# Kernel tuning notes

Hardware: AMD Instinct MI355X
Metric: run time of the kernel (lower is better)

The kernel has to match this reference:

```python
import jax, jax.numpy as jnp
import numpy as np

N_RAYS, N_SAMPLES = 65536, 128


def setup_inputs() -> dict:
    key = jax.random.key(0)
    ks = jax.random.split(key, 6)
    sdf = jax.random.normal(ks[0], (N_RAYS, N_SAMPLES), dtype=jnp.float32)
    color = jax.random.uniform(ks[1], (N_RAYS, N_SAMPLES, 3), dtype=jnp.float32)
    # strictly increasing positive depths per ray
    dz = jax.random.uniform(ks[2], (N_RAYS, N_SAMPLES), dtype=jnp.float32) * 0.05 + 0.01
    z_vals = 0.1 + jnp.cumsum(dz, axis=-1)
    grad_theta = jax.random.normal(ks[3], (N_RAYS, N_SAMPLES, 3), dtype=jnp.float32)
    rd = jax.random.normal(ks[4], (N_RAYS, 3), dtype=jnp.float32)
    rays_d = rd / jnp.linalg.norm(rd, axis=-1, keepdims=True)
    s = jnp.array([64.0], dtype=jnp.float32)  # inv_s from SingleVarianceNetwork
    cos_anneal_ratio = jnp.float32(0.5)
    return {"sdf": sdf, "color": color, "z_vals": z_vals,
            "grad_theta": grad_theta, "rays_d": rays_d, "s": s,
            "cos_anneal_ratio": cos_anneal_ratio}


def reference(sdf, color, z_vals, grad_theta, rays_d, s, cos_anneal_ratio):
    # true cosine between ray dir and SDF gradient: [N, S]
    true_cos = jnp.sum(rays_d[:, None, :] * grad_theta, axis=-1)
    # annealed non-positive cosine (NeuS cos annealing)
    iter_cos = -(jax.nn.relu(-true_cos * 0.5 + 0.5) * (1.0 - cos_anneal_ratio)
                 + jax.nn.relu(-true_cos) * cos_anneal_ratio)
    dists = z_vals[:, 1:] - z_vals[:, :-1]                 # [N, S-1]
    est_next_sdf = sdf[..., :-1] + iter_cos[..., :-1] * dists * 0.5
    est_prev_sdf = sdf[..., :-1] - iter_cos[..., :-1] * dists * 0.5
    sv = s.reshape(())                                     # scalar inv_s
    prev_cdf = jax.nn.sigmoid(est_prev_sdf * sv)
    next_cdf = jax.nn.sigmoid(est_next_sdf * sv)
    alpha = jnp.clip((prev_cdf - next_cdf + 1e-5) / (prev_cdf + 1e-5), 0.0, 1.0)
    transmittance = jnp.cumprod(1.0 - alpha, axis=-1)      # [N, S-1]
    # faithful to source: a ZERO column is prepended to transmittance
    zcol = jnp.zeros((transmittance.shape[0], 1), transmittance.dtype)
    transmittance = jnp.concatenate([zcol, transmittance], axis=-1)  # [N, S]
    alpha = jnp.clip(jnp.concatenate([alpha, zcol], axis=-1), 0.0, 1.0)
    weight = transmittance * alpha                          # [N, S]
    pixel = jnp.sum(weight[..., None] * color, axis=-2)     # [N, 3]
    invdepth = jnp.sum(weight / z_vals, axis=-1)            # [N]
    return pixel, invdepth, weight
```

## Files before the change

### kernel.cpp

```cpp
#include <hip/hip_runtime.h>

#define N_RAYS 65536
#define N_SAMPLES 128
#define RPB 8

__device__ __forceinline__ void gll16(const float* g, float* l) {
    __builtin_amdgcn_global_load_lds(
        (const __attribute__((address_space(1))) void*)g,
        (__attribute__((address_space(3))) void*)l,
        16, 0, 0);
}

__device__ __forceinline__ float sigmoidf(float x) {
    return __fdividef(1.0f, 1.0f + __expf(-x));
}

__global__ __launch_bounds__(256, 8) void neus_kernel(
    const float* __restrict__ sdf,
    const float* __restrict__ color,
    const float* __restrict__ z_vals,
    const float* __restrict__ grad_theta,
    const float* __restrict__ rays_d,
    const float* __restrict__ s_ptr,
    const float* __restrict__ car_ptr,
    float* __restrict__ out_pixel,
    float* __restrict__ out_invdepth,
    float* __restrict__ out_weight)
{
    __shared__ __align__(16) float lds[RPB * N_SAMPLES * 3];

    const int tid = threadIdx.x;
    const int l   = tid & 31;
    const int r   = tid >> 5;
    const int wv  = tid >> 6;
    const int l64 = tid & 63;
    const int ray = blockIdx.x * RPB + r;

    const size_t base  = (size_t)ray * N_SAMPLES;
    const size_t base3 = (size_t)blockIdx.x * (RPB * N_SAMPLES * 3);

    {
        const float* g = grad_theta + base3;
        #pragma unroll
        for (int k = 0; k < 3; ++k) {
            const int q = wv * 3 + k;
            gll16(g + q * 256 + l64 * 4, &lds[q * 256]);
        }
    }

    const float4 sd = *(const float4*)(sdf    + base + 4 * l);
    const float4 zz = *(const float4*)(z_vals + base + 4 * l);
    const float rdx = rays_d[ray * 3 + 0];
    const float rdy = rays_d[ray * 3 + 1];
    const float rdz = rays_d[ray * 3 + 2];
    const float sv  = s_ptr[0];
    const float car = car_ptr[0];
    const float omc = 1.0f - car;

    asm volatile("s_waitcnt vmcnt(0)" ::: "memory");

    const int fo = r * 384 + 12 * l;
    const float4 gA = *(const float4*)&lds[fo + 0];
    const float4 gB = *(const float4*)&lds[fo + 4];
    const float4 gC = *(const float4*)&lds[fo + 8];

    asm volatile("s_waitcnt lgkmcnt(0)" ::: "memory");

    {
        const float* c = color + base3;
        #pragma unroll
        for (int k = 0; k < 3; ++k) {
            const int q = wv * 3 + k;
            gll16(c + q * 256 + l64 * 4, &lds[q * 256]);
        }
    }

    const float tc0 = rdx * gA.x + rdy * gA.y + rdz * gA.z;
    const float tc1 = rdx * gA.w + rdy * gB.x + rdz * gB.y;
    const float tc2 = rdx * gB.z + rdy * gB.w + rdz * gC.x;
    const float tc3 = rdx * gC.y + rdy * gC.z + rdz * gC.w;

    auto iter_cos = [&](float tc) -> float {
        float a = fmaxf(fmaf(tc, -0.5f, 0.5f), 0.0f);
        float b = fmaxf(-tc, 0.0f);
        return -(a * omc + b * car);
    };
    const float ic0 = iter_cos(tc0);
    const float ic1 = iter_cos(tc1);
    const float ic2 = iter_cos(tc2);
    const float ic3 = iter_cos(tc3);

    const float zn = __shfl_down(zz.x, 1, 32);
    const float d0 = zz.y - zz.x;
    const float d1 = zz.z - zz.y;
    const float d2 = zz.w - zz.z;
    const float d3 = zn   - zz.w;

    auto alpha_f = [&](float sdv, float ic, float d) -> float {
        float h  = ic * d * 0.5f;
        float pc = sigmoidf((sdv - h) * sv);
        float nc = sigmoidf((sdv + h) * sv);
        float a  = __fdividef(pc - nc + 1e-5f, pc + 1e-5f);
        return fminf(fmaxf(a, 0.0f), 1.0f);
    };
    const float a0 = alpha_f(sd.x, ic0, d0);
    const float a1 = alpha_f(sd.y, ic1, d1);
    const float a2 = alpha_f(sd.z, ic2, d2);
    const float a3 = (l == 31) ? 0.0f : alpha_f(sd.w, ic3, d3);

    const float om0 = 1.0f - a0;
    const float om1 = 1.0f - a1;
    const float om2 = 1.0f - a2;
    const float om3 = 1.0f - a3;

    float scan = om0 * om1 * om2 * om3;
    #pragma unroll
    for (int off = 1; off < 32; off <<= 1) {
        float v = __shfl_up(scan, off, 32);
        if (l >= off) scan *= v;
    }
    float excl = __shfl_up(scan, 1, 32);
    if (l == 0) excl = 1.0f;

    float t  = excl;
    const float w0 = (l == 0) ? 0.0f : t * a0;
    t *= om0; const float w1 = t * a1;
    t *= om1; const float w2 = t * a2;
    t *= om2; const float w3 = t * a3;

    float inv = w0 * __fdividef(1.0f, zz.x) + w1 * __fdividef(1.0f, zz.y)
              + w2 * __fdividef(1.0f, zz.z) + w3 * __fdividef(1.0f, zz.w);

    asm volatile("s_waitcnt vmcnt(0)" ::: "memory");

    const float4 cA = *(const float4*)&lds[fo + 0];
    const float4 cB = *(const float4*)&lds[fo + 4];
    const float4 cC = *(const float4*)&lds[fo + 8];

    *(float4*)(out_weight + base + 4 * l) = make_float4(w0, w1, w2, w3);

    float pr = w0 * cA.x + w1 * cA.w + w2 * cB.z + w3 * cC.y;
    float pg = w0 * cA.y + w1 * cB.x + w2 * cB.w + w3 * cC.z;
    float pb = w0 * cA.z + w1 * cB.y + w2 * cC.x + w3 * cC.w;

    #pragma unroll
    for (int off = 16; off > 0; off >>= 1) {
        pr  += __shfl_xor(pr,  off, 32);
        pg  += __shfl_xor(pg,  off, 32);
        pb  += __shfl_xor(pb,  off, 32);
        inv += __shfl_xor(inv, off, 32);
    }

    if (l == 0) {
        out_pixel[ray * 3 + 0] = pr;
        out_pixel[ray * 3 + 1] = pg;
        out_pixel[ray * 3 + 2] = pb;
        out_invdepth[ray]      = inv;
    }
}

extern "C" void kernel_launch(void* const* d_in, const int* in_sizes, int n_in,
                              void* d_out, int out_size, void* d_ws, size_t ws_size,
                              hipStream_t stream) {
    const float* sdf        = (const float*)d_in[0];
    const float* color      = (const float*)d_in[1];
    const float* z_vals     = (const float*)d_in[2];
    const float* grad_theta = (const float*)d_in[3];
    const float* rays_d     = (const float*)d_in[4];
    const float* s_ptr      = (const float*)d_in[5];
    const float* car_ptr    = (const float*)d_in[6];

    float* out          = (float*)d_out;
    float* out_pixel    = out;
    float* out_invdepth = out + (size_t)N_RAYS * 3;
    float* out_weight   = out + (size_t)N_RAYS * 4;

    dim3 block(256);
    dim3 grid(N_RAYS / RPB);

    neus_kernel<<<grid, block, 0, stream>>>(
        sdf, color, z_vals, grad_theta, rays_d, s_ptr, car_ptr,
        out_pixel, out_invdepth, out_weight);
}
```

Baseline: 273.8 us.

## Convert to persistent grid with double-buffered LDS prefetch of grad and color

Replaces the one-block-per-8-rays launch with a fixed grid of 768 persistent blocks that loop over ray tiles. While one tile is computed, the next tile's grad_theta and color are prefetched into a second LDS buffer, along with its sdf and z_vals in registers. rays_d is staged into LDS once up front. This aims to hide global-load latency behind compute, at the cost of lower occupancy (launch bounds drop to 3 blocks) and a larger LDS footprint. Fast divisions are also swapped for regular IEEE divisions, which adds ALU cost.

Result: slower. 283.0 us (+3.4%).

```diff
diff --git a/kernel.cpp b/kernel.cpp
--- a/kernel.cpp
+++ b/kernel.cpp
@@ -1,8 +1,12 @@
 #include <hip/hip_runtime.h>
 
-#define N_RAYS 65536
+#define N_RAYS   65536
 #define N_SAMPLES 128
-#define RPB 8
+#define RPT      8
+#define GRID     768
+#define NTG      (N_RAYS / RPT)
+#define MAXT     ((NTG + GRID - 1) / GRID)
+#define TILE_F   (RPT * N_SAMPLES * 3)
 
 __device__ __forceinline__ void gll16(const float* g, float* l) {
     __builtin_amdgcn_global_load_lds(
@@ -12,10 +16,23 @@
 }
 
 __device__ __forceinline__ float sigmoidf(float x) {
-    return __fdividef(1.0f, 1.0f + __expf(-x));
-}
-
-__global__ __launch_bounds__(256, 8) void neus_kernel(
+    return 1.0f / (1.0f + __expf(-x));
+}
+
+__device__ __forceinline__ void stage(const float* __restrict__ grad,
+                                      const float* __restrict__ color,
+                                      float* b, int wv, int l64, size_t rayb) {
+    const float* g = grad  + rayb * (N_SAMPLES * 3);
+    const float* c = color + rayb * (N_SAMPLES * 3);
+    #pragma unroll
+    for (int k = 0; k < 3; ++k) {
+        const int q = wv * 3 + k;
+        gll16(g + (size_t)q * 256 + l64 * 4, b + q * 256);
+        gll16(c + (size_t)q * 256 + l64 * 4, b + TILE_F + q * 256);
+    }
+}
+
+__global__ __launch_bounds__(256, 3) void neus_kernel(
     const float* __restrict__ sdf,
     const float* __restrict__ color,
     const float* __restrict__ z_vals,
@@ -27,135 +44,143 @@
     float* __restrict__ out_invdepth,
     float* __restrict__ out_weight)
 {
-    __shared__ __align__(16) float lds[RPB * N_SAMPLES * 3];
+    __shared__ __align__(16) float buf[2][TILE_F * 2];
+    __shared__ float lds_rd[MAXT * RPT * 3];
 
     const int tid = threadIdx.x;
     const int l   = tid & 31;
-    const int r   = tid >> 5;
+    const int rl  = tid >> 5;
     const int wv  = tid >> 6;
     const int l64 = tid & 63;
-    const int ray = blockIdx.x * RPB + r;
-
-    const size_t base  = (size_t)ray * N_SAMPLES;
-    const size_t base3 = (size_t)blockIdx.x * (RPB * N_SAMPLES * 3);
-
-    {
-        const float* g = grad_theta + base3;
-        #pragma unroll
-        for (int k = 0; k < 3; ++k) {
-            const int q = wv * 3 + k;
-            gll16(g + q * 256 + l64 * 4, &lds[q * 256]);
-        }
+    const int bid = blockIdx.x;
+
+    const int ntiles = (NTG - bid + GRID - 1) / GRID;
+
+    const int nrd = ntiles * RPT * 3;
+    for (int k = tid; k < nrd; k += 256) {
+        const int it  = k / 24;
+        const int rem = k - it * 24;
+        lds_rd[k] = rays_d[(size_t)(bid + it * GRID) * 24 + rem];
     }
 
-    const float4 sd = *(const float4*)(sdf    + base + 4 * l);
-    const float4 zz = *(const float4*)(z_vals + base + 4 * l);
-    const float rdx = rays_d[ray * 3 + 0];
-    const float rdy = rays_d[ray * 3 + 1];
-    const float rdz = rays_d[ray * 3 + 2];
     const float sv  = s_ptr[0];
     const float car = car_ptr[0];
     const float omc = 1.0f - car;
 
-    asm volatile("s_waitcnt vmcnt(0)" ::: "memory");
-
-    const int fo = r * 384 + 12 * l;
-    const float4 gA = *(const float4*)&lds[fo + 0];
-    const float4 gB = *(const float4*)&lds[fo + 4];
-    const float4 gC = *(const float4*)&lds[fo + 8];
-
-    asm volatile("s_waitcnt lgkmcnt(0)" ::: "memory");
-
-    {
-        const float* c = color + base3;
+    __syncthreads();
+
+    size_t tg = bid;
+    int parity = 0;
+    stage(grad_theta, color, buf[0], wv, l64, tg * RPT);
+    float4 sdP = *(const float4*)(sdf    + (tg * RPT + rl) * N_SAMPLES + 4 * l);
+    float4 zzP = *(const float4*)(z_vals + (tg * RPT + rl) * N_SAMPLES + 4 * l);
+
+    for (int i = 0; ; ++i) {
+        const size_t tg_next = tg + GRID;
+        const bool   more    = (i + 1) < ntiles;
+        float4 sdN, zzN;
+        if (more) {
+            stage(grad_theta, color, buf[parity ^ 1], wv, l64, tg_next * RPT);
+            sdN = *(const float4*)(sdf    + (tg_next * RPT + rl) * N_SAMPLES + 4 * l);
+            zzN = *(const float4*)(z_vals + (tg_next * RPT + rl) * N_SAMPLES + 4 * l);
+            asm volatile("s_waitcnt vmcnt(8)" ::: "memory");
+        } else {
+            asm volatile("s_waitcnt vmcnt(0)" ::: "memory");
+        }
+
+        const float* bb = buf[parity];
+        const int fo = rl * 384 + 12 * l;
+        const float4 gA = *(const float4*)(bb + fo);
+        const float4 gB = *(const float4*)(bb + fo + 4);
+        const float4 gC = *(const float4*)(bb + fo + 8);
+        const float4 cA = *(const float4*)(bb + TILE_F + fo);
+        const float4 cB = *(const float4*)(bb + TILE_F + fo + 4);
+        const float4 cC = *(const float4*)(bb + TILE_F + fo + 8);
+        const float rdx = lds_rd[i * 24 + rl * 3 + 0];
+        const float rdy = lds_rd[i * 24 + rl * 3 + 1];
+        const float rdz = lds_rd[i * 24 + rl * 3 + 2];
+        asm volatile("s_waitcnt lgkmcnt(0)" ::: "memory");
+
+        const float tc0 = rdx * gA.x + rdy * gA.y + rdz * gA.z;
+        const float tc1 = rdx * gA.w + rdy * gB.x + rdz * gB.y;
+        const float tc2 = rdx * gB.z + rdy * gB.w + rdz * gC.x;
+        const float tc3 = rdx * gC.y + rdy * gC.z + rdz * gC.w;
+
+        auto iter_cos = [&](float tc) -> float {
+            float a = fmaxf(fmaf(tc, -0.5f, 0.5f), 0.0f);
+            float b = fmaxf(-tc, 0.0f);
+            return -(a * omc + b * car);
+        };
+        const float ic0 = iter_cos(tc0);
+        const float ic1 = iter_cos(tc1);
+        const float ic2 = iter_cos(tc2);
+        const float ic3 = iter_cos(tc3);
+
+        const float zn = __shfl_down(zzP.x, 1, 32);
+        const float d0 = zzP.y - zzP.x;
+        const float d1 = zzP.z - zzP.y;
+        const float d2 = zzP.w - zzP.z;
+        const float d3 = zn    - zzP.w;
+
+        auto alpha_f = [&](float sdv, float ic, float d) -> float {
+            float h  = ic * d * 0.5f;
+            float pc = sigmoidf((sdv - h) * sv);
+            float nc = sigmoidf((sdv + h) * sv);
+            float a  = (pc - nc + 1e-5f) / (pc + 1e-5f);
+            return fminf(fmaxf(a, 0.0f), 1.0f);
+        };
+        const float a0 = alpha_f(sdP.x, ic0, d0);
+        const float a1 = alpha_f(sdP.y, ic1, d1);
+        const float a2 = alpha_f(sdP.z, ic2, d2);
+        const float a3 = (l == 31) ? 0.0f : alpha_f(sdP.w, ic3, d3);
+
+        const float om0 = 1.0f - a0;
+        const float om1 = 1.0f - a1;
+        const float om2 = 1.0f - a2;
+        const float om3 = 1.0f - a3;
+
+        float scan = om0 * om1 * om2 * om3;
         #pragma unroll
-        for (int k = 0; k < 3; ++k) {
-            const int q = wv * 3 + k;
-            gll16(c + q * 256 + l64 * 4, &lds[q * 256]);
-        }
-    }
-
-    const float tc0 = rdx * gA.x + rdy * gA.y + rdz * gA.z;
-    const float tc1 = rdx * gA.w + rdy * gB.x + rdz * gB.y;
-    const float tc2 = rdx * gB.z + rdy * gB.w + rdz * gC.x;
-    const float tc3 = rdx * gC.y + rdy * gC.z + rdz * gC.w;
-
-    auto iter_cos = [&](float tc) -> float {
-        float a = fmaxf(fmaf(tc, -0.5f, 0.5f), 0.0f);
-        float b = fmaxf(-tc, 0.0f);
-        return -(a * omc + b * car);
-    };
-    const float ic0 = iter_cos(tc0);
-    const float ic1 = iter_cos(tc1);
-    const float ic2 = iter_cos(tc2);
-    const float ic3 = iter_cos(tc3);
-
-    const float zn = __shfl_down(zz.x, 1, 32);
-    const float d0 = zz.y - zz.x;
-    const float d1 = zz.z - zz.y;
-    const float d2 = zz.w - zz.z;
-    const float d3 = zn   - zz.w;
-
-    auto alpha_f = [&](float sdv, float ic, float d) -> float {
-        float h  = ic * d * 0.5f;
-        float pc = sigmoidf((sdv - h) * sv);
-        float nc = sigmoidf((sdv + h) * sv);
-        float a  = __fdividef(pc - nc + 1e-5f, pc + 1e-5f);
-        return fminf(fmaxf(a, 0.0f), 1.0f);
-    };
-    const float a0 = alpha_f(sd.x, ic0, d0);
-    const float a1 = alpha_f(sd.y, ic1, d1);
-    const float a2 = alpha_f(sd.z, ic2, d2);
-    const float a3 = (l == 31) ? 0.0f : alpha_f(sd.w, ic3, d3);
-
-    const float om0 = 1.0f - a0;
-    const float om1 = 1.0f - a1;
-    const float om2 = 1.0f - a2;
-    const float om3 = 1.0f - a3;
-
-    float scan = om0 * om1 * om2 * om3;
-    #pragma unroll
-    for (int off = 1; off < 32; off <<= 1) {
-        float v = __shfl_up(scan, off, 32);
-        if (l >= off) scan *= v;
-    }
-    float excl = __shfl_up(scan, 1, 32);
-    if (l == 0) excl = 1.0f;
-
-    float t  = excl;
-    const float w0 = (l == 0) ? 0.0f : t * a0;
-    t *= om0; const float w1 = t * a1;
-    t *= om1; const float w2 = t * a2;
-    t *= om2; const float w3 = t * a3;
-
-    float inv = w0 * __fdividef(1.0f, zz.x) + w1 * __fdividef(1.0f, zz.y)
-              + w2 * __fdividef(1.0f, zz.z) + w3 * __fdividef(1.0f, zz.w);
-
-    asm volatile("s_waitcnt vmcnt(0)" ::: "memory");
-
-    const float4 cA = *(const float4*)&lds[fo + 0];
-    const float4 cB = *(const float4*)&lds[fo + 4];
-    const float4 cC = *(const float4*)&lds[fo + 8];
-
-    *(float4*)(out_weight + base + 4 * l) = make_float4(w0, w1, w2, w3);
-
-    float pr = w0 * cA.x + w1 * cA.w + w2 * cB.z + w3 * cC.y;
-    float pg = w0 * cA.y + w1 * cB.x + w2 * cB.w + w3 * cC.z;
-    float pb = w0 * cA.z + w1 * cB.y + w2 * cC.x + w3 * cC.w;
-
-    #pragma unroll
-    for (int off = 16; off > 0; off >>= 1) {
-        pr  += __shfl_xor(pr,  off, 32);
-        pg  += __shfl_xor(pg,  off, 32);
-        pb  += __shfl_xor(pb,  off, 32);
-        inv += __shfl_xor(inv, off, 32);
-    }
-
-    if (l == 0) {
-        out_pixel[ray * 3 + 0] = pr;
-        out_pixel[ray * 3 + 1] = pg;
-        out_pixel[ray * 3 + 2] = pb;
-        out_invdepth[ray]      = inv;
+        for (int off = 1; off < 32; off <<= 1) {
+            float v = __shfl_up(scan, off, 32);
+            if (l >= off) scan *= v;
+        }
+        float excl = __shfl_up(scan, 1, 32);
+        if (l == 0) excl = 1.0f;
+
+        float t  = excl;
+        const float w0 = (l == 0) ? 0.0f : t * a0;
+        t *= om0; const float w1 = t * a1;
+        t *= om1; const float w2 = t * a2;
+        t *= om2; const float w3 = t * a3;
+
+        float inv = w0 / zzP.x + w1 / zzP.y + w2 / zzP.z + w3 / zzP.w;
+
+        const size_t ray  = tg * RPT + rl;
+        const size_t base = ray * N_SAMPLES;
+        *(float4*)(out_weight + base + 4 * l) = make_float4(w0, w1, w2, w3);
+
+        float pr = w0 * cA.x + w1 * cA.w + w2 * cB.z + w3 * cC.y;
+        float pg = w0 * cA.y + w1 * cB.x + w2 * cB.w + w3 * cC.z;
+        float pb = w0 * cA.z + w1 * cB.y + w2 * cC.x + w3 * cC.w;
+
+        #pragma unroll
+        for (int off = 16; off > 0; off >>= 1) {
+            pr  += __shfl_xor(pr,  off, 32);
+            pg  += __shfl_xor(pg,  off, 32);
+            pb  += __shfl_xor(pb,  off, 32);
+            inv += __shfl_xor(inv, off, 32);
+        }
+
+        if (l == 0) {
+            out_pixel[ray * 3 + 0] = pr;
+            out_pixel[ray * 3 + 1] = pg;
+            out_pixel[ray * 3 + 2] = pb;
+            out_invdepth[ray]      = inv;
+        }
+
+        if (!more) break;
+        sdP = sdN; zzP = zzN; tg = tg_next; parity ^= 1;
     }
 }
 
@@ -176,7 +201,7 @@
     float* out_weight   = out + (size_t)N_RAYS * 4;
 
     dim3 block(256);
-    dim3 grid(N_RAYS / RPB);
+    dim3 grid(GRID);
 
     neus_kernel<<<grid, block, 0, stream>>>(
         sdf, color, z_vals, grad_theta, rays_d, s_ptr, car_ptr,
```

## Replace LDS-staged global_load_lds with direct vector loads of grad and color

Applied to the files above, without the earlier changes.

Drops the LDS staging of grad_theta and color, along with the explicit waitcnt barriers. Each lane now issues three 16-byte global loads directly from its own 48-byte segment, and grad_theta uses nontemporal loads. All loads are issued up front, so color traffic overlaps the compute. The launch-bounds occupancy hint is removed, and fast divides are swapped for IEEE divides, which adds ALU cost. Direct per-lane loads of a 48-byte stride are less coalesced per instruction than the contiguous LDS copy.

Measured after the change: 261.9 us. -4.3%, faster.

```diff
diff --git a/kernel.cpp b/kernel.cpp
--- a/kernel.cpp
+++ b/kernel.cpp
@@ -1,21 +1,22 @@
 #include <hip/hip_runtime.h>
 
-#define N_RAYS 65536
+#define N_RAYS   65536
 #define N_SAMPLES 128
-#define RPB 8
 
-__device__ __forceinline__ void gll16(const float* g, float* l) {
-    __builtin_amdgcn_global_load_lds(
-        (const __attribute__((address_space(1))) void*)g,
-        (__attribute__((address_space(3))) void*)l,
-        16, 0, 0);
+typedef float f4 __attribute__((ext_vector_type(4)));
+
+__device__ __forceinline__ f4 ntload4(const float* p) {
+    return __builtin_nontemporal_load((const f4*)p);
+}
+__device__ __forceinline__ f4 load4(const float* p) {
+    return *(const f4*)p;
 }
 
 __device__ __forceinline__ float sigmoidf(float x) {
-    return __fdividef(1.0f, 1.0f + __expf(-x));
+    return 1.0f / (1.0f + __expf(-x));
 }
 
-__global__ __launch_bounds__(256, 8) void neus_kernel(
+__global__ __launch_bounds__(256) void neus_kernel(
     const float* __restrict__ sdf,
     const float* __restrict__ color,
     const float* __restrict__ z_vals,
@@ -27,53 +28,31 @@
     float* __restrict__ out_invdepth,
     float* __restrict__ out_weight)
 {
-    __shared__ __align__(16) float lds[RPB * N_SAMPLES * 3];
-
     const int tid = threadIdx.x;
     const int l   = tid & 31;
-    const int r   = tid >> 5;
-    const int wv  = tid >> 6;
-    const int l64 = tid & 63;
-    const int ray = blockIdx.x * RPB + r;
+    const int rl  = tid >> 5;
+    const int ray = blockIdx.x * 8 + rl;
 
-    const size_t base  = (size_t)ray * N_SAMPLES;
-    const size_t base3 = (size_t)blockIdx.x * (RPB * N_SAMPLES * 3);
+    const size_t base = (size_t)ray * N_SAMPLES;
+    const size_t b3   = base * 3 + 12 * l;
 
-    {
-        const float* g = grad_theta + base3;
-        #pragma unroll
-        for (int k = 0; k < 3; ++k) {
-            const int q = wv * 3 + k;
-            gll16(g + q * 256 + l64 * 4, &lds[q * 256]);
-        }
-    }
+    const f4 sd = load4(sdf    + base + 4 * l);
+    const f4 zz = load4(z_vals + base + 4 * l);
 
-    const float4 sd = *(const float4*)(sdf    + base + 4 * l);
-    const float4 zz = *(const float4*)(z_vals + base + 4 * l);
+    const f4 gA = ntload4(grad_theta + b3);
+    const f4 gB = ntload4(grad_theta + b3 + 4);
+    const f4 gC = ntload4(grad_theta + b3 + 8);
+
+    const f4 cA = load4(color + b3);
+    const f4 cB = load4(color + b3 + 4);
+    const f4 cC = load4(color + b3 + 8);
+
     const float rdx = rays_d[ray * 3 + 0];
     const float rdy = rays_d[ray * 3 + 1];
     const float rdz = rays_d[ray * 3 + 2];
     const float sv  = s_ptr[0];
     const float car = car_ptr[0];
     const float omc = 1.0f - car;
-
-    asm volatile("s_waitcnt vmcnt(0)" ::: "memory");
-
-    const int fo = r * 384 + 12 * l;
-    const float4 gA = *(const float4*)&lds[fo + 0];
-    const float4 gB = *(const float4*)&lds[fo + 4];
-    const float4 gC = *(const float4*)&lds[fo + 8];
-
-    asm volatile("s_waitcnt lgkmcnt(0)" ::: "memory");
-
-    {
-        const float* c = color + base3;
-        #pragma unroll
-        for (int k = 0; k < 3; ++k) {
-            const int q = wv * 3 + k;
-            gll16(c + q * 256 + l64 * 4, &lds[q * 256]);
-        }
-    }
 
     const float tc0 = rdx * gA.x + rdy * gA.y + rdz * gA.z;
     const float tc1 = rdx * gA.w + rdy * gB.x + rdz * gB.y;
@@ -100,7 +79,7 @@
         float h  = ic * d * 0.5f;
         float pc = sigmoidf((sdv - h) * sv);
         float nc = sigmoidf((sdv + h) * sv);
-        float a  = __fdividef(pc - nc + 1e-5f, pc + 1e-5f);
+        float a  = (pc - nc + 1e-5f) / (pc + 1e-5f);
         return fminf(fmaxf(a, 0.0f), 1.0f);
     };
     const float a0 = alpha_f(sd.x, ic0, d0);
@@ -128,16 +107,10 @@
     t *= om1; const float w2 = t * a2;
     t *= om2; const float w3 = t * a3;
 
-    float inv = w0 * __fdividef(1.0f, zz.x) + w1 * __fdividef(1.0f, zz.y)
-              + w2 * __fdividef(1.0f, zz.z) + w3 * __fdividef(1.0f, zz.w);
+    float inv = w0 / zz.x + w1 / zz.y + w2 / zz.z + w3 / zz.w;
 
-    asm volatile("s_waitcnt vmcnt(0)" ::: "memory");
-
-    const float4 cA = *(const float4*)&lds[fo + 0];
-    const float4 cB = *(const float4*)&lds[fo + 4];
-    const float4 cC = *(const float4*)&lds[fo + 8];
-
-    *(float4*)(out_weight + base + 4 * l) = make_float4(w0, w1, w2, w3);
+    f4 wv; wv.x = w0; wv.y = w1; wv.z = w2; wv.w = w3;
+    *(f4*)(out_weight + base + 4 * l) = wv;
 
     float pr = w0 * cA.x + w1 * cA.w + w2 * cB.z + w3 * cC.y;
     float pg = w0 * cA.y + w1 * cB.x + w2 * cB.w + w3 * cC.z;
@@ -176,7 +149,7 @@
     float* out_weight   = out + (size_t)N_RAYS * 4;
 
     dim3 block(256);
-    dim3 grid(N_RAYS / RPB);
+    dim3 grid(N_RAYS / 8);
 
     neus_kernel<<<grid, block, 0, stream>>>(
         sdf, color, z_vals, grad_theta, rays_d, s_ptr, car_ptr,
```
